# Kernel optimization log

Measured on AMD Instinct MI355X. Metric: run time of the kernel, lower is better.

Reference implementation:

```python
import jax, jax.numpy as jnp
import numpy as np

IMG = 640
NUM_CLASSES = 80
MAX_MATCHES = 10  # == num_gt (required by the module's one-hot loop broadcast)
ALPHA = 0.5
BETA = 6.0
EPS = 1e-05
KEPS = 1e-07  # keras backend epsilon


def _make_anchor_points():
    pts = []
    for s in (8, 16, 32):
        n = IMG // s
        xs = (jnp.arange(n, dtype=jnp.float32) + 0.5) * s
        gx, gy = jnp.meshgrid(xs, xs, indexing='xy')
        pts.append(jnp.stack([gx, gy], axis=-1).reshape(-1, 2))
    return jnp.concatenate(pts, axis=0)  # [8400, 2]


def setup_inputs() -> dict:
    key = jax.random.key(0)
    ks = jax.random.split(key, 6)
    B, A, C, G = 32, 8400, NUM_CLASSES, 10
    anchors = _make_anchor_points()                                  # [A,2]
    scores = jax.random.uniform(ks[0], (B, A, C), dtype=jnp.float32)
    # predicted boxes roughly centered on anchors
    ctr = anchors[None] + 8.0 * jax.random.normal(ks[1], (B, A, 2), dtype=jnp.float32)
    wh = 8.0 + 56.0 * jax.random.uniform(ks[2], (B, A, 2), dtype=jnp.float32)
    decode_bboxes = jnp.concatenate([ctr - wh / 2, ctr + wh / 2], axis=-1)  # [B,A,4]
    # ground-truth boxes (xyxy within image)
    gmin = jax.random.uniform(ks[3], (B, G, 2), dtype=jnp.float32) * (IMG - 170.0)
    gwh = 20.0 + 150.0 * jax.random.uniform(ks[4], (B, G, 2), dtype=jnp.float32)
    gt_bboxes = jnp.concatenate([gmin, gmin + gwh], axis=-1)         # [B,G,4]
    gt_labels = jax.random.randint(ks[5], (B, G), 0, C, dtype=jnp.int32)
    gt_mask = jnp.ones((B, G, 1), dtype=bool)
    return {"scores": scores, "decode_bboxes": decode_bboxes, "anchors": anchors,
            "gt_labels": gt_labels, "gt_bboxes": gt_bboxes, "gt_mask": gt_mask}


def compute_ciou(b1, b2):
    # b1 [B,G,1,4], b2 [B,1,A,4] -> [B,G,A]
    x1a, y1a, x2a, y2a = (b1[..., i] for i in range(4))
    x1b, y1b, x2b, y2b = (b2[..., i] for i in range(4))
    w1 = x2a - x1a
    h1 = y2a - y1a + 1e-05
    w2 = x2b - x1b
    h2 = y2b - y1b + 1e-05
    inter = (jnp.maximum(jnp.minimum(x2a, x2b) - jnp.maximum(x1a, x1b), 0.0) *
             jnp.maximum(jnp.minimum(y2a, y2b) - jnp.maximum(y1a, y1b), 0.0))
    union = w1 * h1 + w2 * h2 - inter + 1e-05
    iou = inter / (union + 1e-05)
    cw = jnp.maximum(x2a, x2b) - jnp.minimum(x1a, x1b)
    ch = jnp.maximum(y2a, y2b) - jnp.minimum(y1a, y1b)
    c2 = cw ** 2 + ch ** 2 + KEPS
    rho2 = (((x1a + x2a) - (x1b + x2b)) / 2) ** 2 + (((y1a + y2a) - (y1b + y2b)) / 2) ** 2
    v = (4.0 / np.pi ** 2) * (jnp.arctan(w2 / h2) - jnp.arctan(w1 / h1)) ** 2
    alpha = v / (v - iou + (1.0 + KEPS))
    return iou - (rho2 / c2 + v * alpha)


def reference(scores, decode_bboxes, anchors, gt_labels, gt_bboxes, gt_mask):
    B, A, C = scores.shape
    G = gt_bboxes.shape[1]
    # per-gt class score for every anchor: [B,G,A]
    idx = jnp.broadcast_to(jnp.maximum(gt_labels, 0)[:, None, :], (B, A, G))
    bbox_scores = jnp.take_along_axis(scores, idx, axis=-1)          # [B,A,G]
    bbox_scores = jnp.transpose(bbox_scores, (0, 2, 1))              # [B,G,A]
    overlaps = compute_ciou(gt_bboxes[:, :, None, :], decode_bboxes[:, None, :, :])  # [B,G,A]
    align = jnp.power(bbox_scores, ALPHA) * jnp.power(overlaps, BETA)
    align = jnp.where(gt_mask, align, 0.0)
    # anchor center strictly inside gt box: [B,G,A]
    in_box = jnp.all((gt_bboxes[:, :, None, :2] < anchors) &
                     (gt_bboxes[:, :, None, 2:] > anchors), axis=-1)
    align = jnp.where(in_box, align, 0.0)
    cand_vals, cand_idxs = jax.lax.top_k(align, MAX_MATCHES)         # [B,G,K]
    cand_idxs = jnp.where(cand_vals > 0, cand_idxs, -1)
    # faithful to original loop: sum_k one_hot(cand_idxs[:, k], A)  -> sum over axis 1
    matched = jax.nn.one_hot(cand_idxs, A, dtype=overlaps.dtype).sum(axis=1)  # [B,K,A]==[B,G,A]
    overlaps = overlaps * matched
    gt_match = jnp.argmax(overlaps, axis=1).astype(jnp.int32)        # [B,A]
    match_mask = jnp.max(overlaps, axis=1) > 0                       # [B,A]
    bbox_labels = jnp.take_along_axis(
        gt_bboxes, jnp.broadcast_to(gt_match[:, :, None], (B, A, 4)), axis=1)  # [B,A,4]
    bbox_labels = jnp.where(match_mask[:, :, None], bbox_labels, -1.0)
    class_labels = jnp.take_along_axis(gt_labels, gt_match, axis=1)  # [B,A]
    class_labels = jnp.where(match_mask, class_labels, -1)
    class_labels = jax.nn.one_hot(class_labels, C, dtype=scores.dtype)  # [B,A,C]
    align = align * matched
    max_align = jnp.max(align, axis=-1, keepdims=True)               # [B,G,1]
    max_overlap = jnp.max(overlaps, axis=-1, keepdims=True)          # [B,G,1]
    norm_align = jnp.max(align * max_overlap / (max_align + EPS), axis=-2)  # [B,A]
    class_labels = class_labels * norm_align[:, :, None]
    fg_mask = (gt_match > -1).astype(jnp.float32)                    # [B,A]
    return (jax.lax.stop_gradient(bbox_labels.reshape(-1, A, 4)),
            jax.lax.stop_gradient(class_labels),
            jax.lax.stop_gradient(fg_mask))
```

## Files before the change

kernel.cpp:

```cpp
#include <hip/hip_runtime.h>
#include <math.h>

#define A_TOT 8400
#define NGT 10
#define NCLS 80
#define KTOP 10
#define NB_BATCH 32
#define CAP 1024

typedef unsigned int u32;
typedef unsigned long long u64;

struct GtP {
    float x1, y1, x2, y2;
    float area1;
    float at1;
    float sx, sy;
    int lab;
    int rawlab;
};

__device__ __forceinline__ void compute_pair(
    const GtP& g,
    float x1b, float y1b, float x2b, float y2b,
    float area2, float at2, float sxb, float syb,
    float ax, float ay, float score,
    float* ciou_out, float* align_out)
{
    float iw = fmaxf(fminf(g.x2, x2b) - fmaxf(g.x1, x1b), 0.0f);
    float ih = fmaxf(fminf(g.y2, y2b) - fmaxf(g.y1, y1b), 0.0f);
    float inter = iw * ih;
    float uni = g.area1 + area2 - inter + 1e-5f;
    float iou = inter / (uni + 1e-5f);
    float cw = fmaxf(g.x2, x2b) - fminf(g.x1, x1b);
    float ch = fmaxf(g.y2, y2b) - fminf(g.y1, y1b);
    float c2 = cw * cw + ch * ch + 1e-7f;
    float dx = (g.sx - sxb) * 0.5f;
    float dy = (g.sy - syb) * 0.5f;
    float rho2 = dx * dx + dy * dy;
    float dat = at2 - g.at1;
    float v = 0.40528473456935109f * (dat * dat);
    float alpha = v / (v - iou + 1.0000001f);
    float o = iou - (rho2 / c2 + v * alpha);
    *ciou_out = o;
    bool inb = (g.x1 < ax) && (g.y1 < ay) && (g.x2 > ax) && (g.y2 > ay);
    float o2 = o * o;
    float p6 = o2 * o2 * o2;
    *align_out = inb ? (sqrtf(score) * p6) : 0.0f;
}

__device__ __forceinline__ void load_gt(const float* gbox, const int* glab, int b, int g, GtP* out)
{
    const float* p = gbox + ((size_t)b * NGT + g) * 4;
    float x1 = p[0], y1 = p[1], x2 = p[2], y2 = p[3];
    out->x1 = x1; out->y1 = y1; out->x2 = x2; out->y2 = y2;
    float w1 = x2 - x1;
    float h1 = y2 - y1 + 1e-5f;
    out->area1 = w1 * h1;
    out->at1 = atanf(w1 / h1);
    out->sx = x1 + x2;
    out->sy = y1 + y2;
    int lb = glab[b * NGT + g];
    out->rawlab = lb;
    out->lab = lb > 0 ? lb : 0;
}

__global__ __launch_bounds__(320) void k_zero(int* __restrict__ counters)
{
    counters[threadIdx.x] = 0;
}

__global__ __launch_bounds__(256) void k_alignfill(
    const float* __restrict__ scores, const float* __restrict__ dec,
    const float* __restrict__ anch, const int* __restrict__ glab,
    const float* __restrict__ gbox,
    u64* __restrict__ entries, int* __restrict__ counters,
    float4* __restrict__ outv)
{
    __shared__ GtP sg[NGT];
    int b = blockIdx.y, tid = threadIdx.x;
    if (tid < NGT) load_gt(gbox, glab, b, tid, &sg[tid]);
    __syncthreads();

    {
        const int NBv = 268800;
        const int NCv = 5644800;
        const int NTv = 5712000;
        int lin = (b * 33 + blockIdx.x) * 256 + tid;
        const int stride = 33 * NB_BATCH * 256;
        for (int i = lin; i < NTv; i += stride) {
            float v = (i < NBv) ? -1.0f : (i < NCv ? 0.0f : 1.0f);
            outv[i] = make_float4(v, v, v, v);
        }
    }

    int a = blockIdx.x * 256 + tid;
    bool valid = (a < A_TOT);
    int asafe = valid ? a : 0;

    float4 bx = ((const float4*)dec)[(size_t)b * A_TOT + asafe];
    float x1b = bx.x, y1b = bx.y, x2b = bx.z, y2b = bx.w;
    float w2 = x2b - x1b;
    float h2 = y2b - y1b + 1e-5f;
    float area2 = w2 * h2;
    float at2 = atanf(w2 / h2);
    float sxb = x1b + x2b, syb = y1b + y2b;
    float2 ap = ((const float2*)anch)[asafe];
    const float* srow = scores + ((size_t)b * A_TOT + asafe) * NCLS;
    int lane = tid & 63;

    #pragma unroll
    for (int g = 0; g < NGT; ++g) {
        bool inb = valid &&
                   (sg[g].x1 < ap.x) && (sg[g].y1 < ap.y) &&
                   (sg[g].x2 > ap.x) && (sg[g].y2 > ap.y);
        float al = 0.0f;
        if (inb) {
            float ci;
            compute_pair(sg[g], x1b, y1b, x2b, y2b, area2, at2, sxb, syb,
                         ap.x, ap.y, srow[sg[g].lab], &ci, &al);
        }
        bool pred = (al > 0.0f);
        u64 mask = __ballot(pred);
        if (mask == 0ull) continue;
        int row = b * NGT + g;
        int leader = __ffsll((long long)mask) - 1;
        int cnt = __popcll(mask);
        int prefix = __popcll(mask & ((1ull << lane) - 1ull));
        int base = 0;
        if (lane == leader) base = atomicAdd(&counters[row], cnt);
        base = __shfl(base, leader, 64);
        int pos = base + prefix;
        if (pred && pos < CAP) {
            u64 key = ((u64)__float_as_uint(al) << 32) | (u32)(~(u32)a);
            entries[(size_t)row * CAP + pos] = key;
        }
    }
}

__device__ __forceinline__ u64 shfl_xor_u64(u64 x, int m)
{
    u32 lo = (u32)x, hi = (u32)(x >> 32);
    lo = __shfl_xor(lo, m, 64);
    hi = __shfl_xor(hi, m, 64);
    return ((u64)hi << 32) | lo;
}

__global__ __launch_bounds__(640) void k_sel(
    const float* __restrict__ scores, const float* __restrict__ dec,
    const float* __restrict__ anch, const int* __restrict__ glab,
    const float* __restrict__ gbox,
    const u64* __restrict__ entries, const int* __restrict__ counters,
    float* __restrict__ out_bbox, float* __restrict__ out_cls)
{
    __shared__ int cid[100];
    __shared__ GtP sg[NGT];
    __shared__ float aLS[NGT][100];
    __shared__ float oLS[NGT][100];
    __shared__ float Cg[NGT];
    int b = blockIdx.x, tid = threadIdx.x;
    int wid = tid >> 6, lane = tid & 63;

    if (tid < NGT) load_gt(gbox, glab, b, tid, &sg[tid]);

    {
        int row = b * NGT + wid;
        int n = counters[row];
        if (n > CAP) n = CAP;
        const u64* e = entries + (size_t)row * CAP;

        u64 L[10];
        #pragma unroll
        for (int j = 0; j < 10; ++j) L[j] = 0ull;
        for (int i = lane; i < n; i += 64) {
            u64 key = e[i];
            if (key > L[9]) {
                L[9] = key;
                #pragma unroll
                for (int j = 9; j > 0; --j) {
                    u64 x = L[j - 1], y = L[j];
                    if (y > x) { L[j - 1] = y; L[j] = x; }
                }
            }
        }
        #pragma unroll
        for (int k = 0; k < KTOP; ++k) {
            u64 c = L[0];
            #pragma unroll
            for (int off = 1; off <= 32; off <<= 1) {
                u64 o = shfl_xor_u64(c, off);
                if (o > c) c = o;
            }
            if (c != 0ull && L[0] == c) {
                #pragma unroll
                for (int j = 0; j < 9; ++j) L[j] = L[j + 1];
                L[9] = 0ull;
            }
            if (lane == 0) {
                int idx = (int)(~(u32)(c & 0xFFFFFFFFu));
                cid[wid * KTOP + k] = (c != 0ull) ? idx : -1;
            }
        }
    }
    __syncthreads();

    for (int t = tid; t < NGT * 100; t += 640) {
        int g = t / 100, e = t - g * 100;
        int a = cid[e];
        float ci = 0.0f, al = 0.0f;
        if (a >= 0) {
            float4 bx = ((const float4*)dec)[(size_t)b * A_TOT + a];
            float x1b = bx.x, y1b = bx.y, x2b = bx.z, y2b = bx.w;
            float w2 = x2b - x1b;
            float h2 = y2b - y1b + 1e-5f;
            float area2 = w2 * h2;
            float at2 = atanf(w2 / h2);
            float2 ap = ((const float2*)anch)[a];
            float s = scores[((size_t)b * A_TOT + a) * NCLS + sg[g].lab];
            compute_pair(sg[g], x1b, y1b, x2b, y2b, area2, at2,
                         x1b + x2b, y1b + y2b, ap.x, ap.y, s, &ci, &al);
        }
        oLS[g][e] = ci;
        aLS[g][e] = al;
    }
    __syncthreads();

    if (tid < NGT) {
        int j = tid;
        float mA = 0.0f, mO = 0.0f;
        for (int gp = 0; gp < NGT; ++gp) {
            int e = gp * NGT + j;
            int a = cid[e];
            if (a < 0) continue;
            int m = 0;
            for (int gq = 0; gq < NGT; ++gq) m += (cid[gq * NGT + j] == a);
            float fm = (float)m;
            mA = fmaxf(mA, aLS[j][e] * fm);
            mO = fmaxf(mO, oLS[j][e] * fm);
        }
        Cg[j] = mO / (mA + 1e-5f);
    }
    __syncthreads();

    if (tid < 100) {
        int e = tid, a = cid[e];
        if (a >= 0) {
            float best = -INFINITY;
            int bg = 0;
            float nrm = 0.0f;
            #pragma unroll
            for (int g = 0; g < NGT; ++g) {
                int m = 0;
                #pragma unroll
                for (int gq = 0; gq < NGT; ++gq) m += (cid[gq * NGT + g] == a);
                float fm = (float)m;
                float vo = oLS[g][e] * fm;
                if (vo > best) { best = vo; bg = g; }
                nrm = fmaxf(nrm, aLS[g][e] * fm * Cg[g]);
            }
            if (best > 0.0f) {
                float4 bb = make_float4(sg[bg].x1, sg[bg].y1, sg[bg].x2, sg[bg].y2);
                ((float4*)out_bbox)[(size_t)b * A_TOT + a] = bb;
                int rl = sg[bg].rawlab;
                if (rl >= 0 && rl < NCLS)
                    out_cls[((size_t)b * A_TOT + a) * NCLS + rl] = nrm;
            }
        }
    }
}

extern "C" void kernel_launch(void* const* d_in, const int* in_sizes, int n_in,
                              void* d_out, int out_size, void* d_ws, size_t ws_size,
                              hipStream_t stream)
{
    (void)in_sizes; (void)n_in; (void)out_size; (void)ws_size;
    const float* scores = (const float*)d_in[0];
    const float* dec    = (const float*)d_in[1];
    const float* anch   = (const float*)d_in[2];
    const int*   glab   = (const int*)d_in[3];
    const float* gbox   = (const float*)d_in[4];

    float* out      = (float*)d_out;
    float* out_bbox = out;
    float* out_cls  = out + (size_t)NB_BATCH * A_TOT * 4;

    int* counters = (int*)d_ws;
    u64* entries  = (u64*)((char*)d_ws + 4096);

    k_zero     <<<1, 320, 0, stream>>>(counters);
    k_alignfill<<<dim3(33, NB_BATCH), 256, 0, stream>>>(scores, dec, anch, glab, gbox,
                                                        entries, counters, (float4*)d_out);
    k_sel      <<<NB_BATCH, 640, 0, stream>>>(scores, dec, anch, glab, gbox,
                                              entries, counters, out_bbox, out_cls);
}
```

Measured before the change: 178.4 us.

## Replace atomic candidate lists with per-wave top-k slots and drop zero kernel

Each wave now writes its own local top-10 alignment keys per GT into a fixed slot, instead of appending every positive candidate to a shared list through atomics. The selection kernel scans a fixed 1320-key array per row. This removes the counter-zeroing launch, the atomic contention and the CAP truncation risk. In exchange it adds shuffle-based top-k reductions in waves with more than 10 candidates and a fixed-size scan in k_sel that may be longer than before.

```diff
diff --git a/kernel.cpp b/kernel.cpp
--- a/kernel.cpp
+++ b/kernel.cpp
@@ -6,7 +6,8 @@
 #define NCLS 80
 #define KTOP 10
 #define NB_BATCH 32
-#define CAP 1024
+#define NWAVE 132
+#define ROWKEYS (NWAVE * KTOP)
 
 typedef unsigned int u32;
 typedef unsigned long long u64;
@@ -65,17 +66,19 @@
     out->lab = lb > 0 ? lb : 0;
 }
 
-__global__ __launch_bounds__(320) void k_zero(int* __restrict__ counters)
-{
-    counters[threadIdx.x] = 0;
+__device__ __forceinline__ u64 shfl_xor_u64(u64 x, int m)
+{
+    u32 lo = (u32)x, hi = (u32)(x >> 32);
+    lo = __shfl_xor(lo, m, 64);
+    hi = __shfl_xor(hi, m, 64);
+    return ((u64)hi << 32) | lo;
 }
 
 __global__ __launch_bounds__(256) void k_alignfill(
     const float* __restrict__ scores, const float* __restrict__ dec,
     const float* __restrict__ anch, const int* __restrict__ glab,
     const float* __restrict__ gbox,
-    u64* __restrict__ entries, int* __restrict__ counters,
-    float4* __restrict__ outv)
+    u64* __restrict__ keys, float4* __restrict__ outv)
 {
     __shared__ GtP sg[NGT];
     int b = blockIdx.y, tid = threadIdx.x;
@@ -97,6 +100,8 @@
     int a = blockIdx.x * 256 + tid;
     bool valid = (a < A_TOT);
     int asafe = valid ? a : 0;
+    int lane = tid & 63;
+    int wglob = blockIdx.x * 4 + (tid >> 6);
 
     float4 bx = ((const float4*)dec)[(size_t)b * A_TOT + asafe];
     float x1b = bx.x, y1b = bx.y, x2b = bx.z, y2b = bx.w;
@@ -107,7 +112,6 @@
     float sxb = x1b + x2b, syb = y1b + y2b;
     float2 ap = ((const float2*)anch)[asafe];
     const float* srow = scores + ((size_t)b * A_TOT + asafe) * NCLS;
-    int lane = tid & 63;
 
     #pragma unroll
     for (int g = 0; g < NGT; ++g) {
@@ -121,36 +125,36 @@
                          ap.x, ap.y, srow[sg[g].lab], &ci, &al);
         }
         bool pred = (al > 0.0f);
+        u64 key = pred ? (((u64)__float_as_uint(al) << 32) | (u32)(~(u32)a)) : 0ull;
         u64 mask = __ballot(pred);
-        if (mask == 0ull) continue;
-        int row = b * NGT + g;
-        int leader = __ffsll((long long)mask) - 1;
         int cnt = __popcll(mask);
-        int prefix = __popcll(mask & ((1ull << lane) - 1ull));
-        int base = 0;
-        if (lane == leader) base = atomicAdd(&counters[row], cnt);
-        base = __shfl(base, leader, 64);
-        int pos = base + prefix;
-        if (pred && pos < CAP) {
-            u64 key = ((u64)__float_as_uint(al) << 32) | (u32)(~(u32)a);
-            entries[(size_t)row * CAP + pos] = key;
-        }
-    }
-}
-
-__device__ __forceinline__ u64 shfl_xor_u64(u64 x, int m)
-{
-    u32 lo = (u32)x, hi = (u32)(x >> 32);
-    lo = __shfl_xor(lo, m, 64);
-    hi = __shfl_xor(hi, m, 64);
-    return ((u64)hi << 32) | lo;
+        u64* slot = keys + ((size_t)((b * NGT + g) * NWAVE + wglob)) * KTOP;
+        if (cnt <= KTOP) {
+            int rank = __popcll(mask & ((1ull << lane) - 1ull));
+            if (pred) slot[rank] = key;
+            if (lane >= cnt && lane < KTOP) slot[lane] = 0ull;
+        } else {
+            u64 cur = key;
+            #pragma unroll
+            for (int k = 0; k < KTOP; ++k) {
+                u64 c = cur;
+                #pragma unroll
+                for (int off = 1; off <= 32; off <<= 1) {
+                    u64 o = shfl_xor_u64(c, off);
+                    if (o > c) c = o;
+                }
+                if (cur == c) cur = 0ull;
+                if (lane == 0) slot[k] = c;
+            }
+        }
+    }
 }
 
 __global__ __launch_bounds__(640) void k_sel(
     const float* __restrict__ scores, const float* __restrict__ dec,
     const float* __restrict__ anch, const int* __restrict__ glab,
     const float* __restrict__ gbox,
-    const u64* __restrict__ entries, const int* __restrict__ counters,
+    const u64* __restrict__ keys,
     float* __restrict__ out_bbox, float* __restrict__ out_cls)
 {
     __shared__ int cid[100];
@@ -164,15 +168,11 @@
     if (tid < NGT) load_gt(gbox, glab, b, tid, &sg[tid]);
 
     {
-        int row = b * NGT + wid;
-        int n = counters[row];
-        if (n > CAP) n = CAP;
-        const u64* e = entries + (size_t)row * CAP;
-
+        const u64* e = keys + (size_t)(b * NGT + wid) * ROWKEYS;
         u64 L[10];
         #pragma unroll
         for (int j = 0; j < 10; ++j) L[j] = 0ull;
-        for (int i = lane; i < n; i += 64) {
+        for (int i = lane; i < ROWKEYS; i += 64) {
             u64 key = e[i];
             if (key > L[9]) {
                 L[9] = key;
@@ -284,12 +284,10 @@
     float* out_bbox = out;
     float* out_cls  = out + (size_t)NB_BATCH * A_TOT * 4;
 
-    int* counters = (int*)d_ws;
-    u64* entries  = (u64*)((char*)d_ws + 4096);
-
-    k_zero     <<<1, 320, 0, stream>>>(counters);
+    u64* keys = (u64*)d_ws;
+
     k_alignfill<<<dim3(33, NB_BATCH), 256, 0, stream>>>(scores, dec, anch, glab, gbox,
-                                                        entries, counters, (float4*)d_out);
+                                                        keys, (float4*)d_out);
     k_sel      <<<NB_BATCH, 640, 0, stream>>>(scores, dec, anch, glab, gbox,
-                                              entries, counters, out_bbox, out_cls);
-}
+                                              keys, out_bbox, out_cls);
+}
```

Result: slower. 188.9 us (+5.9%).
